# Optimization experiments

Measured on AMD Instinct MI355X. Metric: run time of the kernel, lower is better.

Reference implementation:

```python
import jax, jax.numpy as jnp
import numpy as np

B, S, T = 1024, 512, 48


def setup_inputs() -> dict:
    key = jax.random.key(0)
    k1, k2, k3, k4, k5 = jax.random.split(key, 5)
    feats = jax.random.normal(k1, (B, S, T), dtype=jnp.float32)
    tags = jax.random.randint(k2, (B, S), 0, T)
    mask = jnp.ones((B, S), dtype=bool)
    transitions = jax.random.normal(k3, (T, T), dtype=jnp.float32)
    start_transitions = jax.random.normal(k4, (T,), dtype=jnp.float32)
    stop_transitions = jax.random.normal(k5, (T,), dtype=jnp.float32)
    return dict(feats=feats, tags=tags, mask=mask, transitions=transitions,
                start_transitions=start_transitions, stop_transitions=stop_transitions)


def _crf_nll(feats, transitions, start_transitions, stop_transitions, tags, mask):
    # ----- forward algorithm (log partition) -----
    fv0 = start_transitions + feats[:, 0]                      # (B, T)

    def step(fv, xs):
        feat_t, mask_t = xs                                    # (B, T), (B,)
        # transitions[next, cur]: fv over cur axis (last)
        nxt = jax.nn.logsumexp(fv[:, None, :] + transitions[None, :, :]
                               + feat_t[:, :, None], axis=-1)  # (B, T)
        fv = jnp.where(mask_t[:, None], nxt, fv)
        return fv, None

    feats_t = jnp.swapaxes(feats, 0, 1)                        # (S, B, T)
    fv, _ = jax.lax.scan(step, fv0, (feats_t[1:], mask.T[1:]))
    log_z = jax.nn.logsumexp(fv + stop_transitions, axis=-1)   # (B,)

    # ----- gold path score -----
    emit = jnp.take_along_axis(feats, tags[..., None], axis=2)[..., 0]   # (B, S)
    trans = transitions[tags[:, 1:], tags[:, :-1]]                       # (B, S-1)
    gold = emit[:, 0] + start_transitions[tags[:, 0]]
    gold = gold + jnp.sum(jnp.where(mask[:, 1:], trans + emit[:, 1:], 0.0), axis=1)
    last_idx = mask.astype(jnp.int32).sum(axis=1) - 1                    # (B,)
    last_tag = jnp.take_along_axis(tags, last_idx[:, None], axis=1)[:, 0]
    gold = gold + stop_transitions[last_tag]

    return jnp.mean(log_z - gold)


def reference(feats, tags, mask, transitions, start_transitions, stop_transitions):
    return _crf_nll(feats, transitions, start_transitions, stop_transitions, tags, mask)
```

## Files before the change

### kernel.cpp

```cpp
#include <hip/hip_runtime.h>
#include <hip/hip_bf16.h>
#include <math.h>

#define BB 1024
#define SS 512
#define MID 256
#define TT 48
#define BPW 16
#define FWG 64
#define BWG 64

typedef __attribute__((ext_vector_type(8))) short short8;
typedef __attribute__((ext_vector_type(4))) float f32x4;
typedef __attribute__((ext_vector_type(4))) unsigned u32x4;
typedef __attribute__((ext_vector_type(2))) unsigned u32x2;

__device__ __forceinline__ unsigned short f2bf_u(float x) {
    return __builtin_bit_cast(unsigned short, __float2bfloat16(x));
}
__device__ __forceinline__ unsigned pk_bf16(float lo, float hi) {
    return (unsigned)f2bf_u(lo) | ((unsigned)f2bf_u(hi) << 16);
}
__device__ __forceinline__ short f2bf(float x) { return (short)f2bf_u(x); }

template<int CTRL>
__device__ __forceinline__ float dpp_f(float v) {
    int r = __builtin_amdgcn_update_dpp(0, __builtin_bit_cast(int, v),
                                        CTRL, 0xF, 0xF, true);
    return __builtin_bit_cast(float, r);
}
__device__ __forceinline__ float waveSum(float v) {
    v += dpp_f<0x111>(v);
    v += dpp_f<0x112>(v);
    v += dpp_f<0x114>(v);
    v += dpp_f<0x118>(v);
    v += dpp_f<0x142>(v);
    v += dpp_f<0x143>(v);
    return __builtin_bit_cast(float,
        __builtin_amdgcn_readlane(__builtin_bit_cast(int, v), 63));
}

__global__ __launch_bounds__(64, 1) void crf_main(
    const float* __restrict__ feats, const int* __restrict__ tags,
    const float* __restrict__ trans, const float* __restrict__ startT,
    const float* __restrict__ stopT,
    float* __restrict__ qf, float* __restrict__ cf,
    float* __restrict__ qb, float* __restrict__ cb,
    float* __restrict__ gold)
{
    const int lane = threadIdx.x;

    if (blockIdx.x < FWG + BWG) {
        const bool isF = blockIdx.x < FWG;
        __shared__ unsigned Q[16][28];
        __shared__ int ptab[16];
        const int c = lane & 15;
        const int g = lane >> 4;
        const int bi = isF ? blockIdx.x : (blockIdx.x - FWG);
        const int b0 = bi * BPW;
        const float* fb = feats + (size_t)(b0 + c) * SS * TT;

        int pic;
        {
            if (lane < 16) ptab[lane] = lane;
            const short one = f2bf(1.0f);
            short8 PA, PB;
            #pragma unroll
            for (int j = 0; j < 8; j++) {
                PA[j] = (g == 0) ? one : (short)0;
                PB[j] = f2bf((float)c);
            }
            f32x4 z = {0.f, 0.f, 0.f, 0.f};
            f32x4 PD = __builtin_amdgcn_mfma_f32_16x16x32_bf16(PA, PB, z, 0, 0, 0);
            int piv = (int)(PD[0] * 0.125f + 0.5f);
            piv = piv < 0 ? 0 : (piv > 15 ? 15 : piv);
            if (g == 0) ptab[piv] = c;
            pic = ptab[c];
            pic = pic < 0 ? 0 : (pic > 15 ? 15 : pic);
        }

        short8 Afr[3][2];
        #pragma unroll
        for (int r = 0; r < 3; r++)
            #pragma unroll
            for (int s = 0; s < 2; s++) {
                short8 v;
                #pragma unroll
                for (int j = 0; j < 8; j++) {
                    int k = 8 * g + j + 32 * s;
                    int row = 16 * r + c;
                    float e = (k < TT)
                        ? __expf(isF ? trans[row * TT + k] : trans[k * TT + row])
                        : 0.0f;
                    v[j] = f2bf(e);
                }
                Afr[r][s] = v;
            }

        f32x4 prods[3];
        float c_acc = 0.0f;
        float pend_is = 1.0f, pend_lg = 0.0f;
        f32x4 rA[3], rB[3], rC[3], Ecur[3];

        #define PUBLISH_READ() do {                                          \
            _Pragma("unroll")                                                \
            for (int r = 0; r < 3; r++) {                                    \
                u32x2 w = { pk_bf16(prods[r][0], prods[r][1]),               \
                            pk_bf16(prods[r][2], prods[r][3]) };             \
                *(u32x2*)(&Q[c][8 * r + 2 * g]) = w;                         \
            }                                                                \
            const unsigned* src = &Q[pic][0];                                \
            B0 = __builtin_bit_cast(short8, *(const u32x4*)(src + 4 * g));   \
            if (g < 2)                                                       \
                B1 = __builtin_bit_cast(short8, *(const u32x4*)(src + 16 + 4 * g)); \
            else { u32x4 zz = {0u,0u,0u,0u}; B1 = __builtin_bit_cast(short8, zz); } \
        } while (0)

        #define MEASURE() do {                                               \
            float mx = 0.0f;                                                 \
            _Pragma("unroll")                                                \
            for (int r = 0; r < 3; r++)                                      \
                _Pragma("unroll")                                            \
                for (int j = 0; j < 4; j++) {                                \
                    prods[r][j] = fminf(prods[r][j], 1e30f);                 \
                    mx = fmaxf(mx, prods[r][j]);                             \
                }                                                            \
            mx = fmaxf(mx, __shfl_xor(mx, 16));                              \
            mx = fmaxf(mx, __shfl_xor(mx, 32));                              \
            mx = fminf(fmaxf(mx, 1e-30f), 3e37f);                            \
            pend_is = __builtin_amdgcn_rcpf(mx);                             \
            pend_lg = __logf(mx);                                            \
        } while (0)

        #define FOLD() do {                                                  \
            c_acc += pend_lg;                                                \
            _Pragma("unroll")                                                \
            for (int r = 0; r < 3; r++) Ecur[r] *= pend_is;                  \
        } while (0)

        short8 B0, B1;

        if (isF) {
            {
                f32x4 fv[3];
                #pragma unroll
                for (int r = 0; r < 3; r++) {
                    f32x4 st = *(const f32x4*)(startT + 16 * r + 4 * g);
                    f32x4 f0 = *(const f32x4*)(fb + 16 * r + 4 * g);
                    fv[r] = st + f0;
                }
                float mx = fv[0][0];
                #pragma unroll
                for (int r = 0; r < 3; r++)
                    #pragma unroll
                    for (int j = 0; j < 4; j++) mx = fmaxf(mx, fv[r][j]);
                mx = fmaxf(mx, __shfl_xor(mx, 16));
                mx = fmaxf(mx, __shfl_xor(mx, 32));
                c_acc = mx;
                #pragma unroll
                for (int r = 0; r < 3; r++)
                    #pragma unroll
                    for (int j = 0; j < 4; j++)
                        prods[r][j] = __expf(fv[r][j] - mx);
            }
            PUBLISH_READ();
            #pragma unroll
            for (int r = 0; r < 3; r++) {
                f32x4 r1 = *(const f32x4*)(fb + (size_t)1 * TT + 16 * r + 4 * g);
                rA[r] = *(const f32x4*)(fb + (size_t)2 * TT + 16 * r + 4 * g);
                rB[r] = *(const f32x4*)(fb + (size_t)3 * TT + 16 * r + 4 * g);
                rC[r] = *(const f32x4*)(fb + (size_t)4 * TT + 16 * r + 4 * g);
                f32x4 e;
                #pragma unroll
                for (int j = 0; j < 4; j++) e[j] = __expf(r1[j]);
                Ecur[r] = e;
            }

            #pragma unroll 4
            for (int t = 1; t <= MID; t++) {
                int tl = (t + 4 <= MID) ? t + 4 : MID;
                f32x4 rN[3];
                #pragma unroll
                for (int r = 0; r < 3; r++)
                    rN[r] = *(const f32x4*)(fb + (size_t)tl * TT + 16 * r + 4 * g);

                f32x4 D[3];
                #pragma unroll
                for (int r = 0; r < 3; r++) {
                    f32x4 z = {0.f, 0.f, 0.f, 0.f};
                    z = __builtin_amdgcn_mfma_f32_16x16x32_bf16(Afr[r][0], B0, z, 0, 0, 0);
                    z = __builtin_amdgcn_mfma_f32_16x16x32_bf16(Afr[r][1], B1, z, 0, 0, 0);
                    D[r] = z;
                }
                if ((t & 3) == 1) FOLD();
                #pragma unroll
                for (int r = 0; r < 3; r++) prods[r] = D[r] * Ecur[r];
                if ((t & 3) == 0) MEASURE();
                PUBLISH_READ();
                #pragma unroll
                for (int r = 0; r < 3; r++) {
                    f32x4 e;
                    #pragma unroll
                    for (int j = 0; j < 4; j++) e[j] = __expf(rA[r][j]);
                    Ecur[r] = e;
                    rA[r] = rB[r];
                    rB[r] = rC[r];
                    rC[r] = rN[r];
                }
            }
            #pragma unroll
            for (int r = 0; r < 3; r++)
                *(f32x4*)(qf + (size_t)(b0 + c) * TT + 16 * r + 4 * g) = prods[r];
            if (g == 0) cf[b0 + c] = c_acc;
        } else {
            #pragma unroll
            for (int r = 0; r < 3; r++) {
                f32x4 sp = *(const f32x4*)(stopT + 16 * r + 4 * g);
                #pragma unroll
                for (int j = 0; j < 4; j++) prods[r][j] = __expf(sp[j]);
            }
            #pragma unroll
            for (int r = 0; r < 3; r++) {
                f32x4 r1 = *(const f32x4*)(fb + (size_t)(SS - 1) * TT + 16 * r + 4 * g);
                rA[r] = *(const f32x4*)(fb + (size_t)(SS - 2) * TT + 16 * r + 4 * g);
                rB[r] = *(const f32x4*)(fb + (size_t)(SS - 3) * TT + 16 * r + 4 * g);
                rC[r] = *(const f32x4*)(fb + (size_t)(SS - 4) * TT + 16 * r + 4 * g);
                f32x4 e;
                #pragma unroll
                for (int j = 0; j < 4; j++) e[j] = __expf(r1[j]);
                Ecur[r] = e;
            }

            #pragma unroll 4
            for (int t = SS - 1; t >= MID + 1; t--) {
                int tl = (t - 4 >= 0) ? t - 4 : 0;
                f32x4 rN[3];
                #pragma unroll
                for (int r = 0; r < 3; r++)
                    rN[r] = *(const f32x4*)(fb + (size_t)tl * TT + 16 * r + 4 * g);

                if ((t & 3) == 3) FOLD();
                #pragma unroll
                for (int r = 0; r < 3; r++) prods[r] = prods[r] * Ecur[r];
                PUBLISH_READ();
                f32x4 D[3];
                #pragma unroll
                for (int r = 0; r < 3; r++) {
                    f32x4 z = {0.f, 0.f, 0.f, 0.f};
                    z = __builtin_amdgcn_mfma_f32_16x16x32_bf16(Afr[r][0], B0, z, 0, 0, 0);
                    z = __builtin_amdgcn_mfma_f32_16x16x32_bf16(Afr[r][1], B1, z, 0, 0, 0);
                    D[r] = z;
                }
                #pragma unroll
                for (int r = 0; r < 3; r++) prods[r] = D[r];
                if ((t & 3) == 0) MEASURE();
                #pragma unroll
                for (int r = 0; r < 3; r++) {
                    f32x4 e;
                    #pragma unroll
                    for (int j = 0; j < 4; j++) e[j] = __expf(rA[r][j]);
                    Ecur[r] = e;
                    rA[r] = rB[r];
                    rB[r] = rC[r];
                    rC[r] = rN[r];
                }
            }
            #pragma unroll
            for (int r = 0; r < 3; r++)
                *(f32x4*)(qb + (size_t)(b0 + c) * TT + 16 * r + 4 * g) = prods[r];
            if (g == 0) cb[b0 + c] = c_acc;
        }
        #undef PUBLISH_READ
        #undef MEASURE
        #undef FOLD
    } else {
        const int b = blockIdx.x - FWG - BWG;
        const int* tg = tags + b * SS;
        const float* fbg = feats + (size_t)b * SS * TT;
        float acc = 0.0f;
        for (int t = lane; t < SS; t += 64) {
            int cur = tg[t];
            if (t == 0) {
                acc += fbg[cur] + startT[cur];
            } else {
                int prev = tg[t - 1];
                acc += fbg[t * TT + cur] + trans[cur * TT + prev];
            }
        }
        float tot = waveSum(acc);
        if (lane == 0) gold[b] = tot + stopT[tg[SS - 1]];
    }
}

__global__ __launch_bounds__(256) void crf_final(
    const float* __restrict__ qf, const float* __restrict__ cf,
    const float* __restrict__ qb, const float* __restrict__ cb,
    const float* __restrict__ gold, float* __restrict__ out)
{
    __shared__ double sh[256];
    int t = threadIdx.x;
    double s = 0.0;
    for (int b = t * 4; b < t * 4 + 4; b++) {
        float acc = 0.0f;
        for (int j = 0; j < TT; j++)
            acc += qf[(size_t)b * TT + j] * qb[(size_t)b * TT + j];
        acc = fminf(fmaxf(acc, 1e-35f), 3e37f);
        float lz = cf[b] + cb[b] + __logf(acc);
        s += (double)lz - (double)gold[b];
    }
    sh[t] = s;
    __syncthreads();
    for (int ofs = 128; ofs > 0; ofs >>= 1) {
        if (t < ofs) sh[t] += sh[t + ofs];
        __syncthreads();
    }
    if (t == 0) out[0] = (float)(sh[0] / (double)BB);
}

extern "C" void kernel_launch(void* const* d_in, const int* in_sizes, int n_in,
                              void* d_out, int out_size, void* d_ws, size_t ws_size,
                              hipStream_t stream)
{
    const float* feats  = (const float*)d_in[0];
    const int*   tags   = (const int*)d_in[1];
    const float* trans  = (const float*)d_in[3];
    const float* startT = (const float*)d_in[4];
    const float* stopT  = (const float*)d_in[5];

    float* gold = (float*)d_ws;
    float* qf   = gold + BB;
    float* cf   = qf + BB * TT;
    float* qb   = cf + BB;
    float* cb   = qb + BB * TT;

    crf_main<<<FWG + BWG + BB, 64, 0, stream>>>(
        feats, tags, trans, startT, stopT, qf, cf, qb, cb, gold);
    crf_final<<<1, 256, 0, stream>>>(qf, cf, qb, cb, gold, (float*)d_out);
}
```

Baseline: 124.1 us.

## Split CRF sequence into four segments with parallel mid-segment transfer matrices

Rather than one forward and one backward chain each covering half the sequence, the sequence is cut into four 128-step segments. Forward and backward chains cover the outer segments, and 6144 extra single-wave blocks compute the 48x48 transfer matrices of the two middle segments column by column. A prepass converts the exp of the middle feats to bf16 and also computes the gold scores. A combine kernel multiplies the boundary vectors through the bf16 matrices. This shortens the serial critical path by half, at the cost of far more total MFMA work, extra launches, and extra bf16 rounding in the middle matrices.

```diff
diff --git a/kernel.cpp b/kernel.cpp
--- a/kernel.cpp
+++ b/kernel.cpp
@@ -4,11 +4,14 @@
 
 #define BB 1024
 #define SS 512
-#define MID 256
 #define TT 48
-#define BPW 16
-#define FWG 64
-#define BWG 64
+#define T1 128
+#define T2 256
+#define T3 384
+#define GSTEPS 256
+#define NMIDB 6144
+#define MIDBASE 128
+#define CONVB 1024
 
 typedef __attribute__((ext_vector_type(8))) short short8;
 typedef __attribute__((ext_vector_type(4))) float f32x4;
@@ -22,6 +25,15 @@
     return (unsigned)f2bf_u(lo) | ((unsigned)f2bf_u(hi) << 16);
 }
 __device__ __forceinline__ short f2bf(float x) { return (short)f2bf_u(x); }
+
+__device__ __forceinline__ f32x4 unpk4(u32x2 w) {
+    f32x4 e;
+    e[0] = __builtin_bit_cast(float, w[0] << 16);
+    e[1] = __builtin_bit_cast(float, w[0] & 0xffff0000u);
+    e[2] = __builtin_bit_cast(float, w[1] << 16);
+    e[3] = __builtin_bit_cast(float, w[1] & 0xffff0000u);
+    return e;
+}
 
 template<int CTRL>
 __device__ __forceinline__ float dpp_f(float v) {
@@ -40,274 +52,433 @@
         __builtin_amdgcn_readlane(__builtin_bit_cast(int, v), 63));
 }
 
+__device__ __forceinline__ void gold_wave(
+    int b, int lane, const float* feats, const int* tags, const float* trans,
+    const float* startT, const float* stopT, float* gold)
+{
+    const int* tg = tags + b * SS;
+    const float* fbg = feats + (size_t)b * SS * TT;
+    float acc = 0.0f;
+    for (int t = lane; t < SS; t += 64) {
+        int cur = tg[t];
+        if (t == 0) {
+            acc += fbg[cur] + startT[cur];
+        } else {
+            int prev = tg[t - 1];
+            acc += fbg[t * TT + cur] + trans[cur * TT + prev];
+        }
+    }
+    float tot = waveSum(acc);
+    if (lane == 0) gold[b] = tot + stopT[tg[SS - 1]];
+}
+
+__global__ __launch_bounds__(256) void crf_prepass(
+    const float* __restrict__ feats, unsigned short* __restrict__ G,
+    const int* __restrict__ tags, const float* __restrict__ trans,
+    const float* __restrict__ startT, const float* __restrict__ stopT,
+    float* __restrict__ gold)
+{
+    if (blockIdx.x < CONVB) {
+        const int F4B = GSTEPS * TT / 4;
+        const int SRCB = SS * TT / 4;
+        const int SRC0 = (T1 + 1) * TT / 4;
+        const float4* src = (const float4*)feats;
+        ushort4* dst = (ushort4*)G;
+        const int total = BB * F4B;
+        for (int i = blockIdx.x * 256 + threadIdx.x; i < total;
+             i += CONVB * 256) {
+            int b = i / F4B;
+            int r = i - b * F4B;
+            float4 v = src[(size_t)b * SRCB + SRC0 + r];
+            ushort4 o;
+            o.x = f2bf_u(__expf(v.x));
+            o.y = f2bf_u(__expf(v.y));
+            o.z = f2bf_u(__expf(v.z));
+            o.w = f2bf_u(__expf(v.w));
+            dst[i] = o;
+        }
+    } else {
+        const int wv = threadIdx.x >> 6;
+        const int lane = threadIdx.x & 63;
+        gold_wave((blockIdx.x - CONVB) * 4 + wv, lane,
+                  feats, tags, trans, startT, stopT, gold);
+    }
+}
+
 __global__ __launch_bounds__(64, 1) void crf_main(
-    const float* __restrict__ feats, const int* __restrict__ tags,
+    const float* __restrict__ feats, const unsigned short* __restrict__ G,
     const float* __restrict__ trans, const float* __restrict__ startT,
     const float* __restrict__ stopT,
     float* __restrict__ qf, float* __restrict__ cf,
     float* __restrict__ qb, float* __restrict__ cb,
-    float* __restrict__ gold)
+    float* __restrict__ cM, unsigned* __restrict__ Mw)
 {
     const int lane = threadIdx.x;
-
-    if (blockIdx.x < FWG + BWG) {
-        const bool isF = blockIdx.x < FWG;
-        __shared__ unsigned Q[16][28];
-        __shared__ int ptab[16];
-        const int c = lane & 15;
-        const int g = lane >> 4;
-        const int bi = isF ? blockIdx.x : (blockIdx.x - FWG);
-        const int b0 = bi * BPW;
-        const float* fb = feats + (size_t)(b0 + c) * SS * TT;
-
-        int pic;
+    const int role = blockIdx.x < 64 ? 0 : (blockIdx.x < MIDBASE ? 1 : 2);
+    const bool isBwd = (role == 1);
+
+    __shared__ unsigned Q[16][28];
+    __shared__ int ptab[16];
+    const int c = lane & 15;
+    const int g = lane >> 4;
+
+    int b0 = 0, batch = 0, seg = 0, colID = 0;
+    size_t fbIdx = 0;
+    if (role == 2) {
+        int m = blockIdx.x - MIDBASE;
+        batch = m / 6;
+        int rem = m - batch * 6;
+        seg = rem / 3;
+        colID = (rem - seg * 3) * 16 + c;
+        fbIdx = (size_t)batch;
+    } else {
+        int bi = isBwd ? (blockIdx.x - 64) : blockIdx.x;
+        b0 = bi * 16;
+        fbIdx = (size_t)(b0 + c);
+        __builtin_amdgcn_s_setprio(1);
+    }
+    const float* fb = feats + fbIdx * (size_t)(SS * TT);
+
+    int pic;
+    {
+        if (lane < 16) ptab[lane] = lane;
+        const short one = f2bf(1.0f);
+        short8 PA, PB;
+        #pragma unroll
+        for (int j = 0; j < 8; j++) {
+            PA[j] = (g == 0) ? one : (short)0;
+            PB[j] = f2bf((float)c);
+        }
+        f32x4 z = {0.f, 0.f, 0.f, 0.f};
+        f32x4 PD = __builtin_amdgcn_mfma_f32_16x16x32_bf16(PA, PB, z, 0, 0, 0);
+        int piv = (int)(PD[0] * 0.125f + 0.5f);
+        piv = piv < 0 ? 0 : (piv > 15 ? 15 : piv);
+        if (g == 0) ptab[piv] = c;
+        pic = ptab[c];
+        pic = pic < 0 ? 0 : (pic > 15 ? 15 : pic);
+    }
+
+    short8 Afr[3][2];
+    #pragma unroll
+    for (int r = 0; r < 3; r++)
+        #pragma unroll
+        for (int s = 0; s < 2; s++) {
+            short8 v;
+            #pragma unroll
+            for (int j = 0; j < 8; j++) {
+                int k = 8 * g + j + 32 * s;
+                int row = 16 * r + c;
+                float e = (k < TT)
+                    ? __expf(isBwd ? trans[k * TT + row] : trans[row * TT + k])
+                    : 0.0f;
+                v[j] = f2bf(e);
+            }
+            Afr[r][s] = v;
+        }
+
+    f32x4 prods[3];
+    float c_acc = 0.0f;
+    float pend_is = 1.0f, pend_lg = 0.0f;
+    f32x4 Ecur[3];
+    short8 B0, B1;
+
+    #define PUBLISH_READ() do {                                          \
+        _Pragma("unroll")                                                \
+        for (int r = 0; r < 3; r++) {                                    \
+            u32x2 wd = { pk_bf16(prods[r][0], prods[r][1]),              \
+                         pk_bf16(prods[r][2], prods[r][3]) };            \
+            *(u32x2*)(&Q[c][8 * r + 2 * g]) = wd;                        \
+        }                                                                \
+        const unsigned* src = &Q[pic][0];                                \
+        B0 = __builtin_bit_cast(short8, *(const u32x4*)(src + 4 * g));   \
+        if (g < 2)                                                       \
+            B1 = __builtin_bit_cast(short8, *(const u32x4*)(src + 16 + 4 * g)); \
+        else { u32x4 zz = {0u,0u,0u,0u}; B1 = __builtin_bit_cast(short8, zz); } \
+    } while (0)
+
+    #define MEASURE() do {                                               \
+        float mx = 0.0f;                                                 \
+        _Pragma("unroll")                                                \
+        for (int r = 0; r < 3; r++)                                      \
+            _Pragma("unroll")                                            \
+            for (int j = 0; j < 4; j++) {                                \
+                prods[r][j] = fminf(prods[r][j], 1e30f);                 \
+                mx = fmaxf(mx, prods[r][j]);                             \
+            }                                                            \
+        mx = fmaxf(mx, __shfl_xor(mx, 16));                              \
+        mx = fmaxf(mx, __shfl_xor(mx, 32));                              \
+        mx = fminf(fmaxf(mx, 1e-30f), 3e37f);                            \
+        pend_is = __builtin_amdgcn_rcpf(mx);                             \
+        pend_lg = __logf(mx);                                            \
+    } while (0)
+
+    #define FOLD() do {                                                  \
+        c_acc += pend_lg;                                                \
+        _Pragma("unroll")                                                \
+        for (int r = 0; r < 3; r++) Ecur[r] *= pend_is;                  \
+    } while (0)
+
+    #define FINAL_NORM() do {                                            \
+        float mx = 0.0f;                                                 \
+        _Pragma("unroll")                                                \
+        for (int r = 0; r < 3; r++)                                      \
+            _Pragma("unroll")                                            \
+            for (int j = 0; j < 4; j++) {                                \
+                prods[r][j] = fminf(prods[r][j], 1e30f);                 \
+                mx = fmaxf(mx, prods[r][j]);                             \
+            }                                                            \
+        mx = fmaxf(mx, __shfl_xor(mx, 16));                              \
+        mx = fmaxf(mx, __shfl_xor(mx, 32));                              \
+        mx = fminf(fmaxf(mx, 1e-30f), 3e37f);                            \
+        c_acc += __logf(mx);                                             \
+        float inv = __builtin_amdgcn_rcpf(mx);                           \
+        _Pragma("unroll")                                                \
+        for (int r = 0; r < 3; r++) prods[r] *= inv;                     \
+    } while (0)
+
+    if (role == 0) {
+        f32x4 rA[3], rB[3], rC[3];
         {
-            if (lane < 16) ptab[lane] = lane;
-            const short one = f2bf(1.0f);
-            short8 PA, PB;
-            #pragma unroll
-            for (int j = 0; j < 8; j++) {
-                PA[j] = (g == 0) ? one : (short)0;
-                PB[j] = f2bf((float)c);
-            }
-            f32x4 z = {0.f, 0.f, 0.f, 0.f};
-            f32x4 PD = __builtin_amdgcn_mfma_f32_16x16x32_bf16(PA, PB, z, 0, 0, 0);
-            int piv = (int)(PD[0] * 0.125f + 0.5f);
-            piv = piv < 0 ? 0 : (piv > 15 ? 15 : piv);
-            if (g == 0) ptab[piv] = c;
-            pic = ptab[c];
-            pic = pic < 0 ? 0 : (pic > 15 ? 15 : pic);
-        }
-
-        short8 Afr[3][2];
-        #pragma unroll
-        for (int r = 0; r < 3; r++)
-            #pragma unroll
-            for (int s = 0; s < 2; s++) {
-                short8 v;
+            f32x4 fv[3];
+            #pragma unroll
+            for (int r = 0; r < 3; r++) {
+                f32x4 st = *(const f32x4*)(startT + 16 * r + 4 * g);
+                f32x4 f0 = *(const f32x4*)(fb + 16 * r + 4 * g);
+                fv[r] = st + f0;
+            }
+            float mx = fv[0][0];
+            #pragma unroll
+            for (int r = 0; r < 3; r++)
                 #pragma unroll
-                for (int j = 0; j < 8; j++) {
-                    int k = 8 * g + j + 32 * s;
-                    int row = 16 * r + c;
-                    float e = (k < TT)
-                        ? __expf(isF ? trans[row * TT + k] : trans[k * TT + row])
-                        : 0.0f;
-                    v[j] = f2bf(e);
-                }
-                Afr[r][s] = v;
-            }
-
-        f32x4 prods[3];
-        float c_acc = 0.0f;
-        float pend_is = 1.0f, pend_lg = 0.0f;
-        f32x4 rA[3], rB[3], rC[3], Ecur[3];
-
-        #define PUBLISH_READ() do {                                          \
-            _Pragma("unroll")                                                \
-            for (int r = 0; r < 3; r++) {                                    \
-                u32x2 w = { pk_bf16(prods[r][0], prods[r][1]),               \
-                            pk_bf16(prods[r][2], prods[r][3]) };             \
-                *(u32x2*)(&Q[c][8 * r + 2 * g]) = w;                         \
-            }                                                                \
-            const unsigned* src = &Q[pic][0];                                \
-            B0 = __builtin_bit_cast(short8, *(const u32x4*)(src + 4 * g));   \
-            if (g < 2)                                                       \
-                B1 = __builtin_bit_cast(short8, *(const u32x4*)(src + 16 + 4 * g)); \
-            else { u32x4 zz = {0u,0u,0u,0u}; B1 = __builtin_bit_cast(short8, zz); } \
-        } while (0)
-
-        #define MEASURE() do {                                               \
-            float mx = 0.0f;                                                 \
-            _Pragma("unroll")                                                \
-            for (int r = 0; r < 3; r++)                                      \
-                _Pragma("unroll")                                            \
-                for (int j = 0; j < 4; j++) {                                \
-                    prods[r][j] = fminf(prods[r][j], 1e30f);                 \
-                    mx = fmaxf(mx, prods[r][j]);                             \
-                }                                                            \
-            mx = fmaxf(mx, __shfl_xor(mx, 16));                              \
-            mx = fmaxf(mx, __shfl_xor(mx, 32));                              \
-            mx = fminf(fmaxf(mx, 1e-30f), 3e37f);                            \
-            pend_is = __builtin_amdgcn_rcpf(mx);                             \
-            pend_lg = __logf(mx);                                            \
-        } while (0)
-
-        #define FOLD() do {                                                  \
-            c_acc += pend_lg;                                                \
-            _Pragma("unroll")                                                \
-            for (int r = 0; r < 3; r++) Ecur[r] *= pend_is;                  \
-        } while (0)
-
-        short8 B0, B1;
-
-        if (isF) {
-            {
-                f32x4 fv[3];
+                for (int j = 0; j < 4; j++) mx = fmaxf(mx, fv[r][j]);
+            mx = fmaxf(mx, __shfl_xor(mx, 16));
+            mx = fmaxf(mx, __shfl_xor(mx, 32));
+            c_acc = mx;
+            #pragma unroll
+            for (int r = 0; r < 3; r++)
                 #pragma unroll
-                for (int r = 0; r < 3; r++) {
-                    f32x4 st = *(const f32x4*)(startT + 16 * r + 4 * g);
-                    f32x4 f0 = *(const f32x4*)(fb + 16 * r + 4 * g);
-                    fv[r] = st + f0;
-                }
-                float mx = fv[0][0];
-                #pragma unroll
-                for (int r = 0; r < 3; r++)
-                    #pragma unroll
-                    for (int j = 0; j < 4; j++) mx = fmaxf(mx, fv[r][j]);
-                mx = fmaxf(mx, __shfl_xor(mx, 16));
-                mx = fmaxf(mx, __shfl_xor(mx, 32));
-                c_acc = mx;
-                #pragma unroll
-                for (int r = 0; r < 3; r++)
-                    #pragma unroll
-                    for (int j = 0; j < 4; j++)
-                        prods[r][j] = __expf(fv[r][j] - mx);
-            }
+                for (int j = 0; j < 4; j++)
+                    prods[r][j] = __expf(fv[r][j] - mx);
+        }
+        PUBLISH_READ();
+        #pragma unroll
+        for (int r = 0; r < 3; r++) {
+            f32x4 r1 = *(const f32x4*)(fb + (size_t)1 * TT + 16 * r + 4 * g);
+            rA[r] = *(const f32x4*)(fb + (size_t)2 * TT + 16 * r + 4 * g);
+            rB[r] = *(const f32x4*)(fb + (size_t)3 * TT + 16 * r + 4 * g);
+            rC[r] = *(const f32x4*)(fb + (size_t)4 * TT + 16 * r + 4 * g);
+            f32x4 e;
+            #pragma unroll
+            for (int j = 0; j < 4; j++) e[j] = __expf(r1[j]);
+            Ecur[r] = e;
+        }
+        #pragma unroll 4
+        for (int t = 1; t <= T1; t++) {
+            int tl = (t + 4 <= T1) ? t + 4 : T1;
+            f32x4 rN[3];
+            #pragma unroll
+            for (int r = 0; r < 3; r++)
+                rN[r] = *(const f32x4*)(fb + (size_t)tl * TT + 16 * r + 4 * g);
+            f32x4 D[3];
+            #pragma unroll
+            for (int r = 0; r < 3; r++) {
+                f32x4 z = {0.f, 0.f, 0.f, 0.f};
+                z = __builtin_amdgcn_mfma_f32_16x16x32_bf16(Afr[r][0], B0, z, 0, 0, 0);
+                z = __builtin_amdgcn_mfma_f32_16x16x32_bf16(Afr[r][1], B1, z, 0, 0, 0);
+                D[r] = z;
+            }
+            if ((t & 3) == 1) FOLD();
+            #pragma unroll
+            for (int r = 0; r < 3; r++) prods[r] = D[r] * Ecur[r];
+            if ((t & 3) == 0) MEASURE();
             PUBLISH_READ();
             #pragma unroll
             for (int r = 0; r < 3; r++) {
-                f32x4 r1 = *(const f32x4*)(fb + (size_t)1 * TT + 16 * r + 4 * g);
-                rA[r] = *(const f32x4*)(fb + (size_t)2 * TT + 16 * r + 4 * g);
-                rB[r] = *(const f32x4*)(fb + (size_t)3 * TT + 16 * r + 4 * g);
-                rC[r] = *(const f32x4*)(fb + (size_t)4 * TT + 16 * r + 4 * g);
                 f32x4 e;
                 #pragma unroll
-                for (int j = 0; j < 4; j++) e[j] = __expf(r1[j]);
+                for (int j = 0; j < 4; j++) e[j] = __expf(rA[r][j]);
                 Ecur[r] = e;
-            }
-
-            #pragma unroll 4
-            for (int t = 1; t <= MID; t++) {
-                int tl = (t + 4 <= MID) ? t + 4 : MID;
-                f32x4 rN[3];
-                #pragma unroll
-                for (int r = 0; r < 3; r++)
-                    rN[r] = *(const f32x4*)(fb + (size_t)tl * TT + 16 * r + 4 * g);
-
-                f32x4 D[3];
-                #pragma unroll
-                for (int r = 0; r < 3; r++) {
-                    f32x4 z = {0.f, 0.f, 0.f, 0.f};
-                    z = __builtin_amdgcn_mfma_f32_16x16x32_bf16(Afr[r][0], B0, z, 0, 0, 0);
-                    z = __builtin_amdgcn_mfma_f32_16x16x32_bf16(Afr[r][1], B1, z, 0, 0, 0);
-                    D[r] = z;
-                }
-                if ((t & 3) == 1) FOLD();
-                #pragma unroll
-                for (int r = 0; r < 3; r++) prods[r] = D[r] * Ecur[r];
-                if ((t & 3) == 0) MEASURE();
-                PUBLISH_READ();
-                #pragma unroll
-                for (int r = 0; r < 3; r++) {
-                    f32x4 e;
-                    #pragma unroll
-                    for (int j = 0; j < 4; j++) e[j] = __expf(rA[r][j]);
-                    Ecur[r] = e;
-                    rA[r] = rB[r];
-                    rB[r] = rC[r];
-                    rC[r] = rN[r];
-                }
-            }
+                rA[r] = rB[r]; rB[r] = rC[r]; rC[r] = rN[r];
+            }
+        }
+        FINAL_NORM();
+        #pragma unroll
+        for (int r = 0; r < 3; r++)
+            *(f32x4*)(qf + (size_t)(b0 + c) * TT + 16 * r + 4 * g) = prods[r];
+        if (g == 0) cf[b0 + c] = c_acc;
+    } else if (role == 1) {
+        f32x4 rA[3], rB[3], rC[3];
+        #pragma unroll
+        for (int r = 0; r < 3; r++) {
+            f32x4 sp = *(const f32x4*)(stopT + 16 * r + 4 * g);
+            #pragma unroll
+            for (int j = 0; j < 4; j++) prods[r][j] = __expf(sp[j]);
+        }
+        #pragma unroll
+        for (int r = 0; r < 3; r++) {
+            f32x4 r1 = *(const f32x4*)(fb + (size_t)(SS - 1) * TT + 16 * r + 4 * g);
+            rA[r] = *(const f32x4*)(fb + (size_t)(SS - 2) * TT + 16 * r + 4 * g);
+            rB[r] = *(const f32x4*)(fb + (size_t)(SS - 3) * TT + 16 * r + 4 * g);
+            rC[r] = *(const f32x4*)(fb + (size_t)(SS - 4) * TT + 16 * r + 4 * g);
+            f32x4 e;
+            #pragma unroll
+            for (int j = 0; j < 4; j++) e[j] = __expf(r1[j]);
+            Ecur[r] = e;
+        }
+        #pragma unroll 4
+        for (int t = SS - 1; t >= T3 + 1; t--) {
+            int tl = (t - 4 >= 0) ? t - 4 : 0;
+            f32x4 rN[3];
             #pragma unroll
             for (int r = 0; r < 3; r++)
-                *(f32x4*)(qf + (size_t)(b0 + c) * TT + 16 * r + 4 * g) = prods[r];
-            if (g == 0) cf[b0 + c] = c_acc;
-        } else {
-            #pragma unroll
-            for (int r = 0; r < 3; r++) {
-                f32x4 sp = *(const f32x4*)(stopT + 16 * r + 4 * g);
-                #pragma unroll
-                for (int j = 0; j < 4; j++) prods[r][j] = __expf(sp[j]);
-            }
-            #pragma unroll
-            for (int r = 0; r < 3; r++) {
-                f32x4 r1 = *(const f32x4*)(fb + (size_t)(SS - 1) * TT + 16 * r + 4 * g);
-                rA[r] = *(const f32x4*)(fb + (size_t)(SS - 2) * TT + 16 * r + 4 * g);
-                rB[r] = *(const f32x4*)(fb + (size_t)(SS - 3) * TT + 16 * r + 4 * g);
-                rC[r] = *(const f32x4*)(fb + (size_t)(SS - 4) * TT + 16 * r + 4 * g);
+                rN[r] = *(const f32x4*)(fb + (size_t)tl * TT + 16 * r + 4 * g);
+            if ((t & 3) == 3) FOLD();
+            #pragma unroll
+            for (int r = 0; r < 3; r++) prods[r] = prods[r] * Ecur[r];
+            PUBLISH_READ();
+            f32x4 D[3];
+            #pragma unroll
+            for (int r = 0; r < 3; r++) {
+                f32x4 z = {0.f, 0.f, 0.f, 0.f};
+                z = __builtin_amdgcn_mfma_f32_16x16x32_bf16(Afr[r][0], B0, z, 0, 0, 0);
+                z = __builtin_amdgcn_mfma_f32_16x16x32_bf16(Afr[r][1], B1, z, 0, 0, 0);
+                D[r] = z;
+            }
+            #pragma unroll
+            for (int r = 0; r < 3; r++) prods[r] = D[r];
+            if ((t & 3) == 0) MEASURE();
+            #pragma unroll
+            for (int r = 0; r < 3; r++) {
                 f32x4 e;
                 #pragma unroll
-                for (int j = 0; j < 4; j++) e[j] = __expf(r1[j]);
+                for (int j = 0; j < 4; j++) e[j] = __expf(rA[r][j]);
                 Ecur[r] = e;
-            }
-
-            #pragma unroll 4
-            for (int t = SS - 1; t >= MID + 1; t--) {
-                int tl = (t - 4 >= 0) ? t - 4 : 0;
-                f32x4 rN[3];
-                #pragma unroll
-                for (int r = 0; r < 3; r++)
-                    rN[r] = *(const f32x4*)(fb + (size_t)tl * TT + 16 * r + 4 * g);
-
-                if ((t & 3) == 3) FOLD();
-                #pragma unroll
-                for (int r = 0; r < 3; r++) prods[r] = prods[r] * Ecur[r];
-                PUBLISH_READ();
-                f32x4 D[3];
-                #pragma unroll
-                for (int r = 0; r < 3; r++) {
-                    f32x4 z = {0.f, 0.f, 0.f, 0.f};
-                    z = __builtin_amdgcn_mfma_f32_16x16x32_bf16(Afr[r][0], B0, z, 0, 0, 0);
-                    z = __builtin_amdgcn_mfma_f32_16x16x32_bf16(Afr[r][1], B1, z, 0, 0, 0);
-                    D[r] = z;
-                }
-                #pragma unroll
-                for (int r = 0; r < 3; r++) prods[r] = D[r];
-                if ((t & 3) == 0) MEASURE();
-                #pragma unroll
-                for (int r = 0; r < 3; r++) {
-                    f32x4 e;
-                    #pragma unroll
-                    for (int j = 0; j < 4; j++) e[j] = __expf(rA[r][j]);
-                    Ecur[r] = e;
-                    rA[r] = rB[r];
-                    rB[r] = rC[r];
-                    rC[r] = rN[r];
-                }
-            }
+                rA[r] = rB[r]; rB[r] = rC[r]; rC[r] = rN[r];
+            }
+        }
+        FINAL_NORM();
+        #pragma unroll
+        for (int r = 0; r < 3; r++)
+            *(f32x4*)(qb + (size_t)(b0 + c) * TT + 16 * r + 4 * g) = prods[r];
+        if (g == 0) cb[b0 + c] = c_acc;
+    } else {
+        const unsigned short* gb = G + (size_t)batch * GSTEPS * TT;
+        const int goff = seg * T1;
+        u32x2 mA[3], mB[3], mC[3];
+        #pragma unroll
+        for (int r = 0; r < 3; r++)
+            #pragma unroll
+            for (int j = 0; j < 4; j++)
+                prods[r][j] = (16 * r + 4 * g + j == colID) ? 1.0f : 0.0f;
+        PUBLISH_READ();
+        #pragma unroll
+        for (int r = 0; r < 3; r++) {
+            u32x2 w0 = *(const u32x2*)(gb + (size_t)(goff + 0) * TT + 16 * r + 4 * g);
+            mA[r] = *(const u32x2*)(gb + (size_t)(goff + 1) * TT + 16 * r + 4 * g);
+            mB[r] = *(const u32x2*)(gb + (size_t)(goff + 2) * TT + 16 * r + 4 * g);
+            mC[r] = *(const u32x2*)(gb + (size_t)(goff + 3) * TT + 16 * r + 4 * g);
+            Ecur[r] = unpk4(w0);
+        }
+        #pragma unroll 4
+        for (int k = 0; k < T1; k++) {
+            int kl = (k + 4 < T1) ? k + 4 : T1 - 1;
+            u32x2 rN[3];
             #pragma unroll
             for (int r = 0; r < 3; r++)
-                *(f32x4*)(qb + (size_t)(b0 + c) * TT + 16 * r + 4 * g) = prods[r];
-            if (g == 0) cb[b0 + c] = c_acc;
-        }
-        #undef PUBLISH_READ
-        #undef MEASURE
-        #undef FOLD
-    } else {
-        const int b = blockIdx.x - FWG - BWG;
-        const int* tg = tags + b * SS;
-        const float* fbg = feats + (size_t)b * SS * TT;
-        float acc = 0.0f;
-        for (int t = lane; t < SS; t += 64) {
-            int cur = tg[t];
-            if (t == 0) {
-                acc += fbg[cur] + startT[cur];
-            } else {
-                int prev = tg[t - 1];
-                acc += fbg[t * TT + cur] + trans[cur * TT + prev];
-            }
-        }
-        float tot = waveSum(acc);
-        if (lane == 0) gold[b] = tot + stopT[tg[SS - 1]];
-    }
-}
-
-__global__ __launch_bounds__(256) void crf_final(
+                rN[r] = *(const u32x2*)(gb + (size_t)(goff + kl) * TT + 16 * r + 4 * g);
+            f32x4 D[3];
+            #pragma unroll
+            for (int r = 0; r < 3; r++) {
+                f32x4 z = {0.f, 0.f, 0.f, 0.f};
+                z = __builtin_amdgcn_mfma_f32_16x16x32_bf16(Afr[r][0], B0, z, 0, 0, 0);
+                z = __builtin_amdgcn_mfma_f32_16x16x32_bf16(Afr[r][1], B1, z, 0, 0, 0);
+                D[r] = z;
+            }
+            if ((k & 3) == 0) FOLD();
+            #pragma unroll
+            for (int r = 0; r < 3; r++) prods[r] = D[r] * Ecur[r];
+            if ((k & 3) == 3) MEASURE();
+            PUBLISH_READ();
+            #pragma unroll
+            for (int r = 0; r < 3; r++) {
+                Ecur[r] = unpk4(mA[r]);
+                mA[r] = mB[r]; mB[r] = mC[r]; mC[r] = rN[r];
+            }
+        }
+        FINAL_NORM();
+        unsigned* Mb = Mw + ((size_t)(batch * 2 + seg) * TT + colID) * 24;
+        #pragma unroll
+        for (int r = 0; r < 3; r++) {
+            Mb[8 * r + 2 * g + 0] = pk_bf16(prods[r][0], prods[r][1]);
+            Mb[8 * r + 2 * g + 1] = pk_bf16(prods[r][2], prods[r][3]);
+        }
+        if (g == 0) cM[(batch * 2 + seg) * TT + colID] = c_acc;
+    }
+    #undef PUBLISH_READ
+    #undef MEASURE
+    #undef FOLD
+    #undef FINAL_NORM
+}
+
+__global__ __launch_bounds__(256) void crf_combine(
     const float* __restrict__ qf, const float* __restrict__ cf,
     const float* __restrict__ qb, const float* __restrict__ cb,
-    const float* __restrict__ gold, float* __restrict__ out)
+    const float* __restrict__ cM, const unsigned* __restrict__ Mw,
+    const float* __restrict__ gold, float* __restrict__ nll)
+{
+    __shared__ float tsh[4][64];
+    const int wv = threadIdx.x >> 6;
+    const int lane = threadIdx.x & 63;
+    const int b = blockIdx.x * 4 + wv;
+    const bool a = lane < TT;
+    const int lc = a ? lane : (TT - 1);
+
+    float vcur = a ? qf[(size_t)b * TT + lane] : 0.0f;
+    float accl = cf[b];
+
+    for (int s = 0; s < 2; s++) {
+        float cMv = a ? cM[((size_t)b * 2 + s) * TT + lane] : -3e38f;
+        float cmax = cMv;
+        #pragma unroll
+        for (int d = 1; d < 64; d <<= 1)
+            cmax = fmaxf(cmax, __shfl_xor(cmax, d));
+        float tv = a ? vcur * __expf(cMv - cmax) : 0.0f;
+        __syncthreads();
+        tsh[wv][lane] = tv;
+        __syncthreads();
+        const unsigned* Ms = Mw + (size_t)(b * 2 + s) * TT * 24;
+        float w = 0.0f;
+        for (int j = 0; j < TT; j++) {
+            unsigned word = Ms[j * 24 + (lc >> 1)];
+            unsigned bits = (lc & 1) ? (word & 0xffff0000u) : (word << 16);
+            w += __builtin_bit_cast(float, bits) * tsh[wv][j];
+        }
+        if (!a) w = 0.0f;
+        float mw = w;
+        #pragma unroll
+        for (int d = 1; d < 64; d <<= 1)
+            mw = fmaxf(mw, __shfl_xor(mw, d));
+        mw = fminf(fmaxf(mw, 1e-30f), 3e37f);
+        vcur = w * __builtin_amdgcn_rcpf(mw);
+        accl += cmax + __logf(mw);
+    }
+
+    float s2 = a ? qb[(size_t)b * TT + lane] * vcur : 0.0f;
+    #pragma unroll
+    for (int d = 1; d < 64; d <<= 1) s2 += __shfl_xor(s2, d);
+    if (lane == 0) {
+        s2 = fminf(fmaxf(s2, 1e-35f), 3e37f);
+        nll[b] = accl + cb[b] + __logf(s2) - gold[b];
+    }
+}
+
+__global__ __launch_bounds__(256) void crf_mean(
+    const float* __restrict__ nll, float* __restrict__ out)
 {
     __shared__ double sh[256];
     int t = threadIdx.x;
     double s = 0.0;
-    for (int b = t * 4; b < t * 4 + 4; b++) {
-        float acc = 0.0f;
-        for (int j = 0; j < TT; j++)
-            acc += qf[(size_t)b * TT + j] * qb[(size_t)b * TT + j];
-        acc = fminf(fmaxf(acc, 1e-35f), 3e37f);
-        float lz = cf[b] + cb[b] + __logf(acc);
-        s += (double)lz - (double)gold[b];
-    }
+    for (int k = t; k < BB; k += 256) s += (double)nll[k];
     sh[t] = s;
     __syncthreads();
     for (int ofs = 128; ofs > 0; ofs >>= 1) {
@@ -332,8 +503,15 @@
     float* cf   = qf + BB * TT;
     float* qb   = cf + BB;
     float* cb   = qb + BB * TT;
-
-    crf_main<<<FWG + BWG + BB, 64, 0, stream>>>(
-        feats, tags, trans, startT, stopT, qf, cf, qb, cb, gold);
-    crf_final<<<1, 256, 0, stream>>>(qf, cf, qb, cb, gold, (float*)d_out);
-}
+    float* cM   = cb + BB;
+    float* nll  = cM + (size_t)BB * 2 * TT;
+    unsigned* Mw = (unsigned*)(nll + BB);
+    unsigned short* G = (unsigned short*)(Mw + (size_t)BB * 2 * TT * 24);
+
+    crf_prepass<<<CONVB + 256, 256, 0, stream>>>(
+        feats, G, tags, trans, startT, stopT, gold);
+    crf_main<<<MIDBASE + NMIDB, 64, 0, stream>>>(
+        feats, G, trans, startT, stopT, qf, cf, qb, cb, cM, Mw);
+    crf_combine<<<BB / 4, 256, 0, stream>>>(qf, cf, qb, cb, cM, Mw, gold, nll);
+    crf_mean<<<1, 256, 0, stream>>>(nll, (float*)d_out);
+}
```

Result: slower. 194.9 us (+57.0%).
